# Kernel tuning notes

Measured on AMD Instinct MI355X. Metric: run time of the kernel, lower is better.

## Reference

```python
import jax, jax.numpy as jnp
import numpy as np

N_NODES = 100000
N_EDGES = 6400000
TOKEN_DIM = 16


def setup_inputs() -> dict:
    key = jax.random.key(0)
    k1, k2, k3, k4, k5 = jax.random.split(key, 5)
    x = jax.random.normal(k1, (N_NODES, 1), dtype=jnp.float32)
    edge_index = jax.random.randint(k2, (2, N_EDGES), 0, N_NODES, dtype=jnp.int64)
    # PyTorch nn.Linear init: U(-1/sqrt(fan_in), 1/sqrt(fan_in)); plain normals are fine for a correctness baseline
    w1 = jax.random.normal(k3, (TOKEN_DIM, 2), dtype=jnp.float32) * (1.0 / np.sqrt(2.0))
    b1 = jnp.zeros((TOKEN_DIM,), dtype=jnp.float32)
    w2 = jax.random.normal(k4, (TOKEN_DIM, TOKEN_DIM), dtype=jnp.float32) * (1.0 / np.sqrt(TOKEN_DIM))
    b2 = jnp.zeros((TOKEN_DIM,), dtype=jnp.float32)
    return {"x": x, "edge_index": edge_index, "w1": w1, "b1": b1, "w2": w2, "b2": b2}


def reference(x, edge_index, w1, b1, w2, b2):
    row, col = edge_index[0], edge_index[1]
    # gather-multiply: bond_e = s_row * s_col, shape [E, 1]
    bond = x[row] * x[col]
    # scatter-add into local_field, shape [N, 1]
    local_field = jax.ops.segment_sum(bond, row, num_segments=x.shape[0])
    feats = jnp.concatenate([x, local_field], axis=1)  # [N, 2]
    h = jax.nn.relu(feats @ w1.T + b1)                  # [N, token_dim]
    tokens = jax.nn.relu(h @ w2.T + b2)                 # [N, token_dim]
    return tokens
```

## Files before the change

### kernel.cpp

```cpp
#include <hip/hip_runtime.h>
#include <hip/hip_bf16.h>

#define TOKEN_DIM 16
#define RANGES 5
#define MAX_RS 20000
#define MAX_C  96
#define NXCD   8

typedef float floatx4 __attribute__((ext_vector_type(4)));

__global__ __launch_bounds__(1024, 8)
void nit_phase1(const int* __restrict__ row, const int* __restrict__ col,
                const float* __restrict__ x,
                unsigned short* __restrict__ partial,
                int N, long long E, int chunkE, int RS, int C) {
    __shared__ float acc[MAX_RS];
    const int b = blockIdx.x;
    const int k = b % NXCD;
    const int s = b / NXCD;
    const int r = s % RANGES;
    const int c = k + NXCD * (s / RANGES);
    if (c >= C) return;

    const int base = r * RS;
    int cnt = N - base; if (cnt > RS) cnt = RS; if (cnt < 0) cnt = 0;
    const int t = threadIdx.x, nt = blockDim.x;

    for (int j = t; j < cnt; j += nt) acc[j] = 0.0f;
    __syncthreads();

    long long i0 = (long long)c * chunkE;
    long long i1 = i0 + chunkE; if (i1 > E) i1 = E;
    long long len = (i1 > i0) ? (i1 - i0) : 0;
    long long ngrp = len >> 3;
    const unsigned ucnt = (unsigned)cnt;

    long long g = t;
    int4 r0a, r1a, c0a, c1a;
    if (g < ngrp) {
        long long idx = i0 + (g << 3);
        r0a = *reinterpret_cast<const int4*>(row + idx);
        r1a = *reinterpret_cast<const int4*>(row + idx + 4);
        c0a = *reinterpret_cast<const int4*>(col + idx);
        c1a = *reinterpret_cast<const int4*>(col + idx + 4);
    }
    while (g < ngrp) {
        const long long gn = g + nt;
        int4 r0b, r1b, c0b, c1b;
        if (gn < ngrp) {
            long long idx = i0 + (gn << 3);
            r0b = *reinterpret_cast<const int4*>(row + idx);
            r1b = *reinterpret_cast<const int4*>(row + idx + 4);
            c0b = *reinterpret_cast<const int4*>(col + idx);
            c1b = *reinterpret_cast<const int4*>(col + idx + 4);
        }
        const unsigned d0 = (unsigned)(r0a.x - base);
        const unsigned d1 = (unsigned)(r0a.y - base);
        const unsigned d2 = (unsigned)(r0a.z - base);
        const unsigned d3 = (unsigned)(r0a.w - base);
        const unsigned d4 = (unsigned)(r1a.x - base);
        const unsigned d5 = (unsigned)(r1a.y - base);
        const unsigned d6 = (unsigned)(r1a.z - base);
        const unsigned d7 = (unsigned)(r1a.w - base);

        float v0, v1, v2, v3, v4, v5, v6, v7;
        if (d0 < ucnt) v0 = x[c0a.x];
        if (d1 < ucnt) v1 = x[c0a.y];
        if (d2 < ucnt) v2 = x[c0a.z];
        if (d3 < ucnt) v3 = x[c0a.w];
        if (d4 < ucnt) v4 = x[c1a.x];
        if (d5 < ucnt) v5 = x[c1a.y];
        if (d6 < ucnt) v6 = x[c1a.z];
        if (d7 < ucnt) v7 = x[c1a.w];
        __builtin_amdgcn_sched_barrier(0);

        if (d0 < ucnt) atomicAdd(&acc[d0], v0);
        if (d1 < ucnt) atomicAdd(&acc[d1], v1);
        if (d2 < ucnt) atomicAdd(&acc[d2], v2);
        if (d3 < ucnt) atomicAdd(&acc[d3], v3);
        if (d4 < ucnt) atomicAdd(&acc[d4], v4);
        if (d5 < ucnt) atomicAdd(&acc[d5], v5);
        if (d6 < ucnt) atomicAdd(&acc[d6], v6);
        if (d7 < ucnt) atomicAdd(&acc[d7], v7);

        r0a = r0b; r1a = r1b; c0a = c0b; c1a = c1b;
        g = gn;
    }
    for (long long idx = i0 + (ngrp << 3) + t; idx < i1; idx += nt) {
        unsigned d = (unsigned)(row[idx] - base);
        if (d < ucnt) atomicAdd(&acc[d], x[col[idx]]);
    }
    __syncthreads();

    unsigned short* dst = partial + (size_t)c * N + base;
    unsigned int* dst2 = reinterpret_cast<unsigned int*>(dst);
    const int cnt2 = cnt >> 1;
    for (int j = t; j < cnt2; j += nt) {
        __hip_bfloat16 ha = __float2bfloat16(acc[2 * j]);
        __hip_bfloat16 hb = __float2bfloat16(acc[2 * j + 1]);
        unsigned int w = (unsigned int)(*reinterpret_cast<unsigned short*>(&ha))
                       | ((unsigned int)(*reinterpret_cast<unsigned short*>(&hb)) << 16);
        dst2[j] = w;
    }
    if ((cnt & 1) && t == 0) {
        __hip_bfloat16 h = __float2bfloat16(acc[cnt - 1]);
        dst[cnt - 1] = *reinterpret_cast<unsigned short*>(&h);
    }
}

__global__ __launch_bounds__(256, 8)
void nit_phase2(const float* __restrict__ x,
                const unsigned short* __restrict__ partial,
                const float* __restrict__ w1, const float* __restrict__ b1,
                const float* __restrict__ w2, const float* __restrict__ b2,
                float* __restrict__ out, int N, int C) {
    __shared__ float sw1[TOKEN_DIM * 2];
    __shared__ float sb1[TOKEN_DIM];
    __shared__ float sw2[TOKEN_DIM * TOKEN_DIM];
    __shared__ float sb2[TOKEN_DIM];
    __shared__ float red[4][256];

    const int t = threadIdx.x;
    sw2[t] = w2[t];
    if (t < TOKEN_DIM * 2) sw1[t] = w1[t];
    if (t < TOKEN_DIM) { sb1[t] = b1[t]; sb2[t] = b2[t]; }

    const int lane = t & 63;
    const int grp  = t >> 6;
    const int node0 = blockIdx.x << 8;
    const int n4 = node0 + (lane << 2);

    float s0 = 0.0f, s1 = 0.0f, s2 = 0.0f, s3 = 0.0f;
    if (n4 + 3 < N) {
        const unsigned short* p = partial + n4;
#pragma unroll 4
        for (int c = grp; c < C; c += 4) {
            uint2 u = *reinterpret_cast<const uint2*>(p + (size_t)c * N);
            s0 += __uint_as_float(u.x << 16);
            s1 += __uint_as_float(u.x & 0xffff0000u);
            s2 += __uint_as_float(u.y << 16);
            s3 += __uint_as_float(u.y & 0xffff0000u);
        }
    } else if (n4 < N) {
        for (int c = grp; c < C; c += 4) {
            const unsigned short* p = partial + (size_t)c * N;
            s0 += __uint_as_float(((unsigned)p[n4]) << 16);
            if (n4 + 1 < N) s1 += __uint_as_float(((unsigned)p[n4 + 1]) << 16);
            if (n4 + 2 < N) s2 += __uint_as_float(((unsigned)p[n4 + 2]) << 16);
        }
    }
    floatx4 sv = { s0, s1, s2, s3 };
    *reinterpret_cast<floatx4*>(&red[grp][lane << 2]) = sv;
    __syncthreads();

    const int n = node0 + t;
    if (n < N) {
        const float ssum = red[0][t] + red[1][t] + red[2][t] + red[3][t];
        const float xv = x[n];
        const float lv = xv * ssum;

        float h[TOKEN_DIM];
#pragma unroll
        for (int j = 0; j < TOKEN_DIM; ++j) {
            float v = fmaf(xv, sw1[2 * j], fmaf(lv, sw1[2 * j + 1], sb1[j]));
            h[j] = v > 0.0f ? v : 0.0f;
        }

        float o[TOKEN_DIM];
#pragma unroll
        for (int j = 0; j < TOKEN_DIM; ++j) {
            float v = sb2[j];
#pragma unroll
            for (int kk = 0; kk < TOKEN_DIM; ++kk)
                v = fmaf(h[kk], sw2[j * TOKEN_DIM + kk], v);
            o[j] = v > 0.0f ? v : 0.0f;
        }

        floatx4* op = reinterpret_cast<floatx4*>(out + (size_t)n * TOKEN_DIM);
#pragma unroll
        for (int j = 0; j < 4; ++j) {
            floatx4 w = { o[4 * j], o[4 * j + 1], o[4 * j + 2], o[4 * j + 3] };
            op[j] = w;
        }
    }
}

extern "C" void kernel_launch(void* const* d_in, const int* in_sizes, int n_in,
                              void* d_out, int out_size, void* d_ws, size_t ws_size,
                              hipStream_t stream) {
    const float* x  = (const float*)d_in[0];
    const int*   ei = (const int*)d_in[1];
    const float* w1 = (const float*)d_in[2];
    const float* b1 = (const float*)d_in[3];
    const float* w2 = (const float*)d_in[4];
    const float* b2 = (const float*)d_in[5];
    float* out = (float*)d_out;

    const int N = in_sizes[0];
    const long long E = in_sizes[1] / 2;
    const int* row = ei;
    const int* col = ei + E;

    long long maxC = (long long)(ws_size / ((size_t)N * sizeof(unsigned short)));
    int C = maxC < 1 ? 1 : (maxC > MAX_C ? MAX_C : (int)maxC);
    int RS = ((N + RANGES - 1) / RANGES + 1) & ~1;
    long long ce = (E + C - 1) / C;
    int chunkE = (int)((ce + 7LL) & ~7LL);

    unsigned short* partial = (unsigned short*)d_ws;

    const int cg = (C + NXCD - 1) / NXCD;
    const int grid1 = NXCD * RANGES * cg;
    nit_phase1<<<grid1, 1024, 0, stream>>>(row, col, x, partial,
                                           N, E, chunkE, RS, C);

    int grid2 = (N + 255) / 256;
    nit_phase2<<<grid2, 256, 0, stream>>>(x, partial, w1, b1, w2, b2,
                                          out, N, C);
}
```

Measured before the change: 147.2 us.

## Fuse scatter and MLP phases into one cooperative kernel with grid sync

Merges the two kernels into a single cooperative launch: blocks first build the per-chunk partial sums, then sync across the whole grid and reuse the same 1024-thread blocks to reduce the partials and run the MLP over node tiles in a grid-stride loop. Phase 2 now splits the chunk reduction across 16 wavefront groups instead of 4. The gather loads are also moved ahead of the next index prefetch. This removes one kernel launch gap and gives more parallel reads per reduction, at the cost of a grid barrier and only 256 of 1024 threads doing the MLP. A non-cooperative two-kernel fallback is kept.

New measurement: 533.3 us. 262% more time.

```diff
diff --git a/kernel.cpp b/kernel.cpp
--- a/kernel.cpp
+++ b/kernel.cpp
@@ -1,21 +1,24 @@
 #include <hip/hip_runtime.h>
 #include <hip/hip_bf16.h>
+#include <hip/hip_cooperative_groups.h>
 
 #define TOKEN_DIM 16
 #define RANGES 5
 #define MAX_RS 20000
 #define MAX_C  96
 #define NXCD   8
+#define P2G    16
 
 typedef float floatx4 __attribute__((ext_vector_type(4)));
 
-__global__ __launch_bounds__(1024, 8)
-void nit_phase1(const int* __restrict__ row, const int* __restrict__ col,
-                const float* __restrict__ x,
-                unsigned short* __restrict__ partial,
-                int N, long long E, int chunkE, int RS, int C) {
-    __shared__ float acc[MAX_RS];
-    const int b = blockIdx.x;
+namespace cg = cooperative_groups;
+
+__device__ __forceinline__
+void phase1_body(float* acc,
+                 const int* __restrict__ row, const int* __restrict__ col,
+                 const float* __restrict__ x, unsigned short* __restrict__ partial,
+                 int N, long long E, int chunkE, int RS, int C, int b) {
+    const int t = threadIdx.x, nt = blockDim.x;
     const int k = b % NXCD;
     const int s = b / NXCD;
     const int r = s % RANGES;
@@ -24,7 +27,7 @@
 
     const int base = r * RS;
     int cnt = N - base; if (cnt > RS) cnt = RS; if (cnt < 0) cnt = 0;
-    const int t = threadIdx.x, nt = blockDim.x;
+    const unsigned ucnt = (unsigned)cnt;
 
     for (int j = t; j < cnt; j += nt) acc[j] = 0.0f;
     __syncthreads();
@@ -33,7 +36,6 @@
     long long i1 = i0 + chunkE; if (i1 > E) i1 = E;
     long long len = (i1 > i0) ? (i1 - i0) : 0;
     long long ngrp = len >> 3;
-    const unsigned ucnt = (unsigned)cnt;
 
     long long g = t;
     int4 r0a, r1a, c0a, c1a;
@@ -45,6 +47,25 @@
         c1a = *reinterpret_cast<const int4*>(col + idx + 4);
     }
     while (g < ngrp) {
+        const unsigned d0 = (unsigned)(r0a.x - base);
+        const unsigned d1 = (unsigned)(r0a.y - base);
+        const unsigned d2 = (unsigned)(r0a.z - base);
+        const unsigned d3 = (unsigned)(r0a.w - base);
+        const unsigned d4 = (unsigned)(r1a.x - base);
+        const unsigned d5 = (unsigned)(r1a.y - base);
+        const unsigned d6 = (unsigned)(r1a.z - base);
+        const unsigned d7 = (unsigned)(r1a.w - base);
+
+        float v0, v1, v2, v3, v4, v5, v6, v7;
+        if (d0 < ucnt) v0 = x[c0a.x];
+        if (d1 < ucnt) v1 = x[c0a.y];
+        if (d2 < ucnt) v2 = x[c0a.z];
+        if (d3 < ucnt) v3 = x[c0a.w];
+        if (d4 < ucnt) v4 = x[c1a.x];
+        if (d5 < ucnt) v5 = x[c1a.y];
+        if (d6 < ucnt) v6 = x[c1a.z];
+        if (d7 < ucnt) v7 = x[c1a.w];
+
         const long long gn = g + nt;
         int4 r0b, r1b, c0b, c1b;
         if (gn < ngrp) {
@@ -54,24 +75,6 @@
             c0b = *reinterpret_cast<const int4*>(col + idx);
             c1b = *reinterpret_cast<const int4*>(col + idx + 4);
         }
-        const unsigned d0 = (unsigned)(r0a.x - base);
-        const unsigned d1 = (unsigned)(r0a.y - base);
-        const unsigned d2 = (unsigned)(r0a.z - base);
-        const unsigned d3 = (unsigned)(r0a.w - base);
-        const unsigned d4 = (unsigned)(r1a.x - base);
-        const unsigned d5 = (unsigned)(r1a.y - base);
-        const unsigned d6 = (unsigned)(r1a.z - base);
-        const unsigned d7 = (unsigned)(r1a.w - base);
-
-        float v0, v1, v2, v3, v4, v5, v6, v7;
-        if (d0 < ucnt) v0 = x[c0a.x];
-        if (d1 < ucnt) v1 = x[c0a.y];
-        if (d2 < ucnt) v2 = x[c0a.z];
-        if (d3 < ucnt) v3 = x[c0a.w];
-        if (d4 < ucnt) v4 = x[c1a.x];
-        if (d5 < ucnt) v5 = x[c1a.y];
-        if (d6 < ucnt) v6 = x[c1a.z];
-        if (d7 < ucnt) v7 = x[c1a.w];
         __builtin_amdgcn_sched_barrier(0);
 
         if (d0 < ucnt) atomicAdd(&acc[d0], v0);
@@ -108,96 +111,133 @@
     }
 }
 
-__global__ __launch_bounds__(256, 8)
-void nit_phase2(const float* __restrict__ x,
-                const unsigned short* __restrict__ partial,
-                const float* __restrict__ w1, const float* __restrict__ b1,
-                const float* __restrict__ w2, const float* __restrict__ b2,
-                float* __restrict__ out, int N, int C) {
-    __shared__ float sw1[TOKEN_DIM * 2];
-    __shared__ float sb1[TOKEN_DIM];
-    __shared__ float sw2[TOKEN_DIM * TOKEN_DIM];
-    __shared__ float sb2[TOKEN_DIM];
-    __shared__ float red[4][256];
-
+__device__ __forceinline__
+void phase2_body(float* lds,
+                 const float* __restrict__ x, const unsigned short* __restrict__ partial,
+                 const float* __restrict__ w1, const float* __restrict__ b1,
+                 const float* __restrict__ w2, const float* __restrict__ b2,
+                 float* __restrict__ out, int N, int C, int b, int gsz) {
     const int t = threadIdx.x;
-    sw2[t] = w2[t];
-    if (t < TOKEN_DIM * 2) sw1[t] = w1[t];
-    if (t < TOKEN_DIM) { sb1[t] = b1[t]; sb2[t] = b2[t]; }
-
-    const int lane = t & 63;
-    const int grp  = t >> 6;
-    const int node0 = blockIdx.x << 8;
-    const int n4 = node0 + (lane << 2);
-
-    float s0 = 0.0f, s1 = 0.0f, s2 = 0.0f, s3 = 0.0f;
-    if (n4 + 3 < N) {
-        const unsigned short* p = partial + n4;
-#pragma unroll 4
-        for (int c = grp; c < C; c += 4) {
-            uint2 u = *reinterpret_cast<const uint2*>(p + (size_t)c * N);
-            s0 += __uint_as_float(u.x << 16);
-            s1 += __uint_as_float(u.x & 0xffff0000u);
-            s2 += __uint_as_float(u.y << 16);
-            s3 += __uint_as_float(u.y & 0xffff0000u);
+    float* red  = lds;
+    float* wbuf = lds + P2G * 256;
+    if (t < 32) wbuf[t] = w1[t];
+    else if (t < 48) wbuf[t] = b1[t - 32];
+    else if (t < 304) wbuf[t] = w2[t - 48];
+    else if (t < 320) wbuf[t] = b2[t - 304];
+
+    const int lane = t & 63, grp = t >> 6;
+    const int ntiles = (N + 255) >> 8;
+    for (int tile = b; tile < ntiles; tile += gsz) {
+        const int node0 = tile << 8;
+        const int n4 = node0 + (lane << 2);
+        float s0 = 0.f, s1 = 0.f, s2 = 0.f, s3 = 0.f;
+        if (n4 + 3 < N) {
+            const unsigned short* p = partial + n4;
+            for (int cc = grp; cc < C; cc += P2G) {
+                uint2 u = *reinterpret_cast<const uint2*>(p + (size_t)cc * N);
+                s0 += __uint_as_float(u.x << 16);
+                s1 += __uint_as_float(u.x & 0xffff0000u);
+                s2 += __uint_as_float(u.y << 16);
+                s3 += __uint_as_float(u.y & 0xffff0000u);
+            }
+        } else if (n4 < N) {
+            for (int cc = grp; cc < C; cc += P2G) {
+                const unsigned short* p = partial + (size_t)cc * N;
+                s0 += __uint_as_float(((unsigned)p[n4]) << 16);
+                if (n4 + 1 < N) s1 += __uint_as_float(((unsigned)p[n4 + 1]) << 16);
+                if (n4 + 2 < N) s2 += __uint_as_float(((unsigned)p[n4 + 2]) << 16);
+            }
         }
-    } else if (n4 < N) {
-        for (int c = grp; c < C; c += 4) {
-            const unsigned short* p = partial + (size_t)c * N;
-            s0 += __uint_as_float(((unsigned)p[n4]) << 16);
-            if (n4 + 1 < N) s1 += __uint_as_float(((unsigned)p[n4 + 1]) << 16);
-            if (n4 + 2 < N) s2 += __uint_as_float(((unsigned)p[n4 + 2]) << 16);
+        __syncthreads();
+        floatx4 sv = { s0, s1, s2, s3 };
+        *reinterpret_cast<floatx4*>(&red[grp * 256 + (lane << 2)]) = sv;
+        __syncthreads();
+
+        if (t < 256) {
+            const int n = node0 + t;
+            if (n < N) {
+                float ssum = 0.f;
+#pragma unroll
+                for (int gi = 0; gi < P2G; ++gi) ssum += red[gi * 256 + t];
+                const float xv = x[n];
+                const float lv = xv * ssum;
+                const float* sw1 = wbuf;
+                const float* sb1 = wbuf + 32;
+                const float* sw2 = wbuf + 48;
+                const float* sb2 = wbuf + 304;
+
+                float h[TOKEN_DIM];
+#pragma unroll
+                for (int j = 0; j < TOKEN_DIM; ++j) {
+                    float v = fmaf(xv, sw1[2 * j], fmaf(lv, sw1[2 * j + 1], sb1[j]));
+                    h[j] = v > 0.0f ? v : 0.0f;
+                }
+                floatx4* op = reinterpret_cast<floatx4*>(out + (size_t)n * TOKEN_DIM);
+#pragma unroll
+                for (int j4 = 0; j4 < 4; ++j4) {
+                    floatx4 o;
+#pragma unroll
+                    for (int jj = 0; jj < 4; ++jj) {
+                        const int j = j4 * 4 + jj;
+                        float v = sb2[j];
+#pragma unroll
+                        for (int kk = 0; kk < TOKEN_DIM; ++kk)
+                            v = fmaf(h[kk], sw2[j * TOKEN_DIM + kk], v);
+                        o[jj] = v > 0.0f ? v : 0.0f;
+                    }
+                    op[j4] = o;
+                }
+            }
         }
     }
-    floatx4 sv = { s0, s1, s2, s3 };
-    *reinterpret_cast<floatx4*>(&red[grp][lane << 2]) = sv;
-    __syncthreads();
-
-    const int n = node0 + t;
-    if (n < N) {
-        const float ssum = red[0][t] + red[1][t] + red[2][t] + red[3][t];
-        const float xv = x[n];
-        const float lv = xv * ssum;
-
-        float h[TOKEN_DIM];
-#pragma unroll
-        for (int j = 0; j < TOKEN_DIM; ++j) {
-            float v = fmaf(xv, sw1[2 * j], fmaf(lv, sw1[2 * j + 1], sb1[j]));
-            h[j] = v > 0.0f ? v : 0.0f;
-        }
-
-        float o[TOKEN_DIM];
-#pragma unroll
-        for (int j = 0; j < TOKEN_DIM; ++j) {
-            float v = sb2[j];
-#pragma unroll
-            for (int kk = 0; kk < TOKEN_DIM; ++kk)
-                v = fmaf(h[kk], sw2[j * TOKEN_DIM + kk], v);
-            o[j] = v > 0.0f ? v : 0.0f;
-        }
-
-        floatx4* op = reinterpret_cast<floatx4*>(out + (size_t)n * TOKEN_DIM);
-#pragma unroll
-        for (int j = 0; j < 4; ++j) {
-            floatx4 w = { o[4 * j], o[4 * j + 1], o[4 * j + 2], o[4 * j + 3] };
-            op[j] = w;
-        }
-    }
+}
+
+__global__ __launch_bounds__(1024, 8)
+void nit_fused(const int* __restrict__ row, const int* __restrict__ col,
+               const float* __restrict__ x, unsigned short* __restrict__ partial,
+               const float* __restrict__ w1, const float* __restrict__ b1,
+               const float* __restrict__ w2, const float* __restrict__ b2,
+               float* __restrict__ out, int N, long long E, int chunkE, int RS, int C) {
+    __shared__ float acc[MAX_RS];
+    phase1_body(acc, row, col, x, partial, N, E, chunkE, RS, C, blockIdx.x);
+
+    __threadfence();
+    cg::this_grid().sync();
+    __threadfence();
+
+    phase2_body(acc, x, partial, w1, b1, w2, b2, out, N, C, blockIdx.x, gridDim.x);
+}
+
+__global__ __launch_bounds__(1024, 8)
+void nit_p1(const int* __restrict__ row, const int* __restrict__ col,
+            const float* __restrict__ x, unsigned short* __restrict__ partial,
+            int N, long long E, int chunkE, int RS, int C) {
+    __shared__ float acc[MAX_RS];
+    phase1_body(acc, row, col, x, partial, N, E, chunkE, RS, C, blockIdx.x);
+}
+
+__global__ __launch_bounds__(1024, 8)
+void nit_p2(const float* __restrict__ x, const unsigned short* __restrict__ partial,
+            const float* __restrict__ w1, const float* __restrict__ b1,
+            const float* __restrict__ w2, const float* __restrict__ b2,
+            float* __restrict__ out, int N, int C) {
+    __shared__ float lds[P2G * 256 + 320];
+    phase2_body(lds, x, partial, w1, b1, w2, b2, out, N, C, blockIdx.x, gridDim.x);
 }
 
 extern "C" void kernel_launch(void* const* d_in, const int* in_sizes, int n_in,
                               void* d_out, int out_size, void* d_ws, size_t ws_size,
                               hipStream_t stream) {
+    const int*   ei = (const int*)d_in[1];
     const float* x  = (const float*)d_in[0];
-    const int*   ei = (const int*)d_in[1];
     const float* w1 = (const float*)d_in[2];
     const float* b1 = (const float*)d_in[3];
     const float* w2 = (const float*)d_in[4];
     const float* b2 = (const float*)d_in[5];
     float* out = (float*)d_out;
 
-    const int N = in_sizes[0];
-    const long long E = in_sizes[1] / 2;
+    int N = in_sizes[0];
+    long long E = in_sizes[1] / 2;
     const int* row = ei;
     const int* col = ei + E;
 
@@ -209,12 +249,17 @@
 
     unsigned short* partial = (unsigned short*)d_ws;
 
-    const int cg = (C + NXCD - 1) / NXCD;
-    const int grid1 = NXCD * RANGES * cg;
-    nit_phase1<<<grid1, 1024, 0, stream>>>(row, col, x, partial,
-                                           N, E, chunkE, RS, C);
-
-    int grid2 = (N + 255) / 256;
-    nit_phase2<<<grid2, 256, 0, stream>>>(x, partial, w1, b1, w2, b2,
-                                          out, N, C);
-}
+    const int cgc = (C + NXCD - 1) / NXCD;
+    int grid1 = NXCD * RANGES * cgc;
+
+    void* args[] = { (void*)&row, (void*)&col, (void*)&x, (void*)&partial,
+                     (void*)&w1, (void*)&b1, (void*)&w2, (void*)&b2, (void*)&out,
+                     (void*)&N, (void*)&E, (void*)&chunkE, (void*)&RS, (void*)&C };
+    hipError_t err = hipLaunchCooperativeKernel((const void*)nit_fused,
+                                                dim3(grid1), dim3(1024),
+                                                args, 0, stream);
+    if (err != hipSuccess) {
+        nit_p1<<<grid1, 1024, 0, stream>>>(row, col, x, partial, N, E, chunkE, RS, C);
+        nit_p2<<<grid1, 1024, 0, stream>>>(x, partial, w1, b1, w2, b2, out, N, C);
+    }
+}
```
